# Kernel optimization log

Measured on AMD Instinct MI355X. Metric: run time of the kernel, lower is better.

Reference implementation:

```python
import jax, jax.numpy as jnp
import numpy as np

N = 100_000   # nodes
E = 1_600_000 # message-passing edges
EA = 1_000_000 # aux edges for bilinear head
G = 512       # graphs in batch
F_IN = 16     # num_node_features (fixed in source)
H = 32        # hidden_dim (fixed in source)


def setup_inputs() -> dict:
    key = jax.random.key(0)
    ks = jax.random.split(key, 8)
    x = jax.random.normal(ks[0], (N, F_IN), jnp.float32)
    edge_index = jax.random.randint(ks[1], (2, E), 0, N, dtype=jnp.int32)
    edge_index_aux = jax.random.randint(ks[2], (2, EA), 0, N, dtype=jnp.int32)
    batch = jnp.sort(jax.random.randint(ks[3], (N,), 0, G, dtype=jnp.int32))
    W1 = jax.random.normal(ks[4], (F_IN, H), jnp.float32) / np.sqrt(F_IN)
    b1 = jnp.zeros((H,), jnp.float32)
    W2 = jax.random.normal(ks[5], (H, H), jnp.float32) / np.sqrt(H)
    b2 = jnp.zeros((H,), jnp.float32)
    Wr = jax.random.normal(ks[6], (H, 1), jnp.float32) / np.sqrt(H)
    br = jnp.zeros((1,), jnp.float32)
    Wbil = jax.random.normal(ks[7], (1, H, H), jnp.float32) / H
    bbil = jnp.zeros((1,), jnp.float32)
    return dict(x=x, edge_index=edge_index, edge_index_aux=edge_index_aux,
                batch=batch, W1=W1, b1=b1, W2=W2, b2=b2, Wr=Wr, br=br,
                Wbil=Wbil, bbil=bbil)


def gcn_conv(x, W, b, src, dst):
    # PyG GCNConv: x' = D^{-1/2}(A+I)D^{-1/2} (x W) + b, deg includes self-loop
    xw = x @ W                                                   # [N,H]
    deg = jax.ops.segment_sum(jnp.ones((src.shape[0],), x.dtype), dst,
                              num_segments=N) + 1.0              # +1 self-loop
    dinv = jax.lax.rsqrt(deg)                                    # [N]
    coef = dinv[src] * dinv[dst]                                 # [E]
    agg = jax.ops.segment_sum(xw[src] * coef[:, None], dst, num_segments=N)
    agg = agg + xw * (dinv * dinv)[:, None]                      # self-loop msg
    return agg + b


def reference(x, edge_index, edge_index_aux, batch,
              W1, b1, W2, b2, Wr, br, Wbil, bbil):
    src, dst = edge_index[0], edge_index[1]
    h = jax.nn.relu(gcn_conv(x, W1, b1, src, dst))
    h = gcn_conv(h, W2, b2, src, dst)
    # global_mean_pool over graph ids
    cnt = jax.ops.segment_sum(jnp.ones((N,), h.dtype), batch, num_segments=G)
    pooled = jax.ops.segment_sum(h, batch, num_segments=G) / jnp.maximum(cnt, 1.0)[:, None]
    reg_output = pooled @ Wr + br                                # [G,1]
    # Bilinear edge head: out_e = x1_e^T W x2_e + b
    h1 = h[edge_index_aux[0]]                                    # [EA,H]
    h2 = h[edge_index_aux[1]]                                    # [EA,H]
    edge_pred = jnp.einsum('ei,ij,ej->e', h1, Wbil[0], h2)[:, None] + bbil
    return reg_output, edge_pred
```

## Files before the change

### kernel.cpp

```cpp
#include <hip/hip_runtime.h>
#include <hip/hip_bf16.h>
#include <string.h>
#include <stdint.h>

typedef __hip_bfloat16 bf16;

#define FIN 16
#define H   32
#define PADW 64
#define NB  512
#define BINCAP 4096
#define NPBMAX 200
#define PSTRIDE 65
#define CHUNK 4096
#define SCAN_CHUNK 1024
#define MAXSEG 64
#define POOLBLK 256

typedef int vi4 __attribute__((ext_vector_type(4)));

__device__ __forceinline__ float b2f(bf16 v) { return __bfloat162float(v); }

__device__ __forceinline__ float loadf(const void* p, size_t i, int f32) {
    return f32 ? ((const float*)p)[i] : b2f(((const bf16*)p)[i]);
}
__device__ __forceinline__ void storef(void* p, size_t i, float v, int f32) {
    if (f32) ((float*)p)[i] = v;
    else     ((bf16*)p)[i] = __float2bfloat16(v);
}

__device__ __forceinline__ unsigned pack2(float lo, float hi) {
    bf16 a = __float2bfloat16(lo), b = __float2bfloat16(hi);
    unsigned short ua, ub;
    memcpy(&ua, &a, 2); memcpy(&ub, &b, 2);
    return ((unsigned)ub << 16) | (unsigned)ua;
}
__device__ __forceinline__ float f_lo(unsigned u) {
    union { unsigned i; float f; } v; v.i = u << 16; return v.f;
}
__device__ __forceinline__ float f_hi(unsigned u) {
    union { unsigned i; float f; } v; v.i = u & 0xffff0000u; return v.f;
}

__global__ void k_detect(const void* __restrict__ x, int nelem, int* __restrict__ flag,
                         float* __restrict__ zf, int nzf,
                         int* __restrict__ zi, int nzi) {
    for (int i = threadIdx.x; i < nzf; i += blockDim.x) zf[i] = 0.f;
    if (zi) for (int i = threadIdx.x; i < nzi; i += blockDim.x) zi[i] = 0;
    __shared__ int cntS;
    if (threadIdx.x == 0) cntS = 0;
    __syncthreads();
    int bad = 0;
    const bf16* p = (const bf16*)x;
    for (int i = threadIdx.x; i < nelem; i += blockDim.x) {
        float v = b2f(p[i]);
        float a = fabsf(v);
        if (isnan(v) || a > 1024.f || (v != 0.f && a < 1e-20f)) bad++;
    }
    atomicAdd(&cntS, bad);
    __syncthreads();
    if (threadIdx.x == 0) flag[0] = (cntS > 64) ? 1 : 0;
}

__global__ void __launch_bounds__(1024) k_p1(
        const int* __restrict__ src, const int* __restrict__ dst,
        int* __restrict__ bincur, unsigned* __restrict__ binbuf,
        int E, int npb) {
    __shared__ int hcnt[4][NB];
    __shared__ int hbase[NB];
    __shared__ int scur[NB];
    int tid = threadIdx.x;
    int grp = tid >> 8;
    int e0 = blockIdx.x * CHUNK;
    int nE = E - e0;
    if (nE > CHUNK) nE = CHUNK;
    for (int i = tid; i < 4 * NB; i += blockDim.x) ((int*)hcnt)[i] = 0;
    __syncthreads();
    for (int i = tid; i < nE; i += blockDim.x)
        atomicAdd(&hcnt[grp][dst[e0 + i] / npb], 1);
    __syncthreads();
    for (int i = tid; i < NB; i += blockDim.x) {
        int c = hcnt[0][i] + hcnt[1][i] + hcnt[2][i] + hcnt[3][i];
        hbase[i] = c ? atomicAdd(&bincur[i], c) : 0;
        scur[i] = 0;
    }
    __syncthreads();
    for (int i = tid; i < nE; i += blockDim.x) {
        int d = dst[e0 + i];
        int bin = d / npb;
        int pos = hbase[bin] + atomicAdd(&scur[bin], 1);
        if (pos < BINCAP)
            binbuf[(size_t)bin * BINCAP + pos] =
                ((unsigned)src[e0 + i] << 10) | (unsigned)(d - bin * npb);
    }
}

__global__ void __launch_bounds__(256) k_p2x(
        const int* __restrict__ bincur, const unsigned* __restrict__ binbuf,
        int* __restrict__ csr, int* __restrict__ deg, float* __restrict__ dinv,
        const void* __restrict__ x, const void* __restrict__ W1,
        const int* __restrict__ flag, unsigned* __restrict__ xsb,
        int N, int npb) {
    __shared__ int cur[NPBMAX];
    __shared__ int psr[NPBMAX * PSTRIDE];
    __shared__ float sW1[FIN * H];
    int f32v = flag[0];
    int b = blockIdx.x;
    int base = b * npb;
    int nn = N - base;
    if (nn > npb) nn = npb;
    if (nn < 0) nn = 0;
    for (int i = threadIdx.x; i < FIN * H; i += blockDim.x) sW1[i] = loadf(W1, i, f32v);
    for (int i = threadIdx.x; i < nn; i += blockDim.x) cur[i] = 0;
    __syncthreads();
    int cnt = bincur[b];
    if (cnt > BINCAP) cnt = BINCAP;
    const unsigned* buf = binbuf + (size_t)b * BINCAP;
    for (int j = threadIdx.x; j < cnt; j += blockDim.x) {
        unsigned p = buf[j];
        int loc = (int)(p & 1023u);
        int s = (int)(p >> 10);
        int pos = atomicAdd(&cur[loc], 1);
        if (pos < PADW) psr[loc * PSTRIDE + pos] = s;
    }
    __syncthreads();
    int tot = nn * PADW;
    for (int idx = threadIdx.x; idx < tot; idx += blockDim.x) {
        int i = idx >> 6, p = idx & 63;
        int dg = cur[i];
        if (dg > PADW) dg = PADW;
        if (p < dg)
            csr[((size_t)(base + i) << 6) + p] = psr[i * PSTRIDE + p];
    }
    for (int i = threadIdx.x; i < nn; i += blockDim.x) {
        int dg = cur[i];
        int n = base + i;
        deg[n] = dg;
        float dv = rsqrtf((float)dg + 1.0f);
        dinv[n] = dv;
        float xr[FIN];
        if (f32v) {
            const float4* xp = (const float4*)((const float*)x + (size_t)n * FIN);
            float4 v0 = xp[0], v1 = xp[1], v2 = xp[2], v3 = xp[3];
            xr[0]=v0.x; xr[1]=v0.y; xr[2]=v0.z; xr[3]=v0.w;
            xr[4]=v1.x; xr[5]=v1.y; xr[6]=v1.z; xr[7]=v1.w;
            xr[8]=v2.x; xr[9]=v2.y; xr[10]=v2.z; xr[11]=v2.w;
            xr[12]=v3.x; xr[13]=v3.y; xr[14]=v3.z; xr[15]=v3.w;
        } else {
            const uint4* xp = (const uint4*)((const bf16*)x + (size_t)n * FIN);
            uint4 u0 = xp[0], u1 = xp[1];
            xr[0]=f_lo(u0.x); xr[1]=f_hi(u0.x); xr[2]=f_lo(u0.y); xr[3]=f_hi(u0.y);
            xr[4]=f_lo(u0.z); xr[5]=f_hi(u0.z); xr[6]=f_lo(u0.w); xr[7]=f_hi(u0.w);
            xr[8]=f_lo(u1.x); xr[9]=f_hi(u1.x); xr[10]=f_lo(u1.y); xr[11]=f_hi(u1.y);
            xr[12]=f_lo(u1.z); xr[13]=f_hi(u1.z); xr[14]=f_lo(u1.w); xr[15]=f_hi(u1.w);
        }
        unsigned outp[16];
#pragma unroll
        for (int jj = 0; jj < 16; jj++) {
            float s0 = 0.f, s1 = 0.f;
#pragma unroll
            for (int f = 0; f < FIN; f++) {
                float xv = xr[f];
                s0 += xv * sW1[f * H + 2 * jj];
                s1 += xv * sW1[f * H + 2 * jj + 1];
            }
            outp[jj] = pack2(s0 * dv, s1 * dv);
        }
        uint4* op = (uint4*)(xsb + (size_t)n * 16);
        op[0] = make_uint4(outp[0], outp[1], outp[2], outp[3]);
        op[1] = make_uint4(outp[4], outp[5], outp[6], outp[7]);
        op[2] = make_uint4(outp[8], outp[9], outp[10], outp[11]);
        op[3] = make_uint4(outp[12], outp[13], outp[14], outp[15]);
    }
}


__global__ void k_fillp(const int* __restrict__ src, const int* __restrict__ dst,
                        int* __restrict__ cursor, int* __restrict__ csr, int E) {
    int e = blockIdx.x * blockDim.x + threadIdx.x;
    if (e >= E) return;
    int d = dst[e];
    int pos = atomicAdd(&cursor[d], 1);
    if (pos < PADW) csr[((size_t)d << 6) + pos] = src[e];
}

__global__ void k_dinvi(const int* __restrict__ deg, float* __restrict__ dinv, int N) {
    int t = blockIdx.x * blockDim.x + threadIdx.x;
    if (t < N) dinv[t] = rsqrtf((float)deg[t] + 1.0f);
}

__global__ void __launch_bounds__(256) k_xw1v(
        const void* __restrict__ x, const void* __restrict__ W1,
        const float* __restrict__ dinv, const int* __restrict__ flag,
        unsigned* __restrict__ xsb, int N) {
    __shared__ float sW[FIN * H];
    __shared__ float sxx[16 * 17];
    int f32 = flag[0];
    for (int i = threadIdx.x; i < FIN * H; i += blockDim.x) sW[i] = loadf(W1, i, f32);
    __syncthreads();
    int t = blockIdx.x * blockDim.x + threadIdx.x;
    int n = t >> 4, j = t & 15, g = threadIdx.x >> 4;
    if (n < N) sxx[g * 17 + j] = loadf(x, (size_t)n * FIN + j, f32);
    __syncthreads();
    if (n >= N) return;
    float dv = dinv[n];
    float s0 = 0.f, s1 = 0.f;
    const float* xp = &sxx[g * 17];
#pragma unroll
    for (int i = 0; i < FIN; i++) {
        float xv = xp[i];
        s0 += xv * sW[i * H + 2 * j];
        s1 += xv * sW[i * H + 2 * j + 1];
    }
    xsb[(size_t)n * 16 + j] = pack2(s0 * dv, s1 * dv);
}

#define GACC8(TBL)                                                        \
    for (; k + 8 <= len; k += 8) {                                        \
        vi4 sA = *(const vi4*)(lst + k);                                  \
        vi4 sB = *(const vi4*)(lst + k + 4);                              \
        unsigned u0 = TBL[(size_t)sA.x * 16 + j];                         \
        unsigned u1 = TBL[(size_t)sA.y * 16 + j];                         \
        unsigned u2 = TBL[(size_t)sA.z * 16 + j];                         \
        unsigned u3 = TBL[(size_t)sA.w * 16 + j];                         \
        unsigned u4 = TBL[(size_t)sB.x * 16 + j];                         \
        unsigned u5 = TBL[(size_t)sB.y * 16 + j];                         \
        unsigned u6 = TBL[(size_t)sB.z * 16 + j];                         \
        unsigned u7 = TBL[(size_t)sB.w * 16 + j];                         \
        a0 += f_lo(u0); a1 += f_hi(u0);                                   \
        b0 += f_lo(u1); b1v += f_hi(u1);                                  \
        a0 += f_lo(u2); a1 += f_hi(u2);                                   \
        b0 += f_lo(u3); b1v += f_hi(u3);                                  \
        a0 += f_lo(u4); a1 += f_hi(u4);                                   \
        b0 += f_lo(u5); b1v += f_hi(u5);                                  \
        a0 += f_lo(u6); a1 += f_hi(u6);                                   \
        b0 += f_lo(u7); b1v += f_hi(u7);                                  \
    }                                                                     \
    for (; k + 4 <= len; k += 4) {                                        \
        vi4 s4 = *(const vi4*)(lst + k);                                  \
        unsigned u0 = TBL[(size_t)s4.x * 16 + j];                         \
        unsigned u1 = TBL[(size_t)s4.y * 16 + j];                         \
        unsigned u2 = TBL[(size_t)s4.z * 16 + j];                         \
        unsigned u3 = TBL[(size_t)s4.w * 16 + j];                         \
        a0 += f_lo(u0); a1 += f_hi(u0);                                   \
        b0 += f_lo(u1); b1v += f_hi(u1);                                  \
        a0 += f_lo(u2); a1 += f_hi(u2);                                   \
        b0 += f_lo(u3); b1v += f_hi(u3);                                  \
    }                                                                     \
    for (; k < len; k++) {                                                \
        unsigned u2 = TBL[(size_t)lst[k] * 16 + j];                       \
        a0 += f_lo(u2); a1 += f_hi(u2);                                   \
    }

__global__ void __launch_bounds__(256) k_g1(
        const int* __restrict__ deg, const int* __restrict__ csr,
        const float* __restrict__ dinv, const unsigned* __restrict__ xsb,
        const void* __restrict__ W2, const void* __restrict__ b1,
        const int* __restrict__ flag, unsigned* __restrict__ xsb2, int N) {
    __shared__ float sW[H * H];
    __shared__ float sb[H];
    __shared__ float shh[16 * 34];
    int f32 = flag[0];
    for (int i = threadIdx.x; i < H * H; i += blockDim.x) sW[i] = loadf(W2, i, f32);
    if (threadIdx.x < H) sb[threadIdx.x] = loadf(b1, threadIdx.x, f32);
    __syncthreads();
    int t = blockIdx.x * blockDim.x + threadIdx.x;
    int d = t >> 4, j = t & 15, g = threadIdx.x >> 4;
    float dv = 0.f;
    if (d < N) {
        int len = deg[d];
        if (len > PADW) len = PADW;
        const int* lst = csr + ((size_t)d << 6);
        unsigned u = xsb[(size_t)d * 16 + j];
        float a0 = f_lo(u), a1 = f_hi(u);
        float b0 = 0.f, b1v = 0.f;
        int k = 0;
        GACC8(xsb)
        dv = dinv[d];
        float h0 = (a0 + b0) * dv + sb[2 * j];
        float h1 = (a1 + b1v) * dv + sb[2 * j + 1];
        shh[g * 34 + 2 * j]     = h0 > 0.f ? h0 : 0.f;
        shh[g * 34 + 2 * j + 1] = h1 > 0.f ? h1 : 0.f;
    }
    __syncthreads();
    if (d >= N) return;
    float s0 = 0.f, s1 = 0.f;
    const float* hp = &shh[g * 34];
#pragma unroll
    for (int i = 0; i < H; i++) {
        float hv = hp[i];
        s0 += hv * sW[i * H + 2 * j];
        s1 += hv * sW[i * H + 2 * j + 1];
    }
    xsb2[(size_t)d * 16 + j] = pack2(s0 * dv, s1 * dv);
}

__global__ void __launch_bounds__(256) k_g2(
        const int* __restrict__ deg, const int* __restrict__ csr,
        const float* __restrict__ dinv, const unsigned* __restrict__ xsb2,
        const void* __restrict__ b2v, const void* __restrict__ Wbil,
        const int* __restrict__ batch, const int* __restrict__ flag,
        float* __restrict__ pooled, float* __restrict__ cnt,
        unsigned* __restrict__ hb, unsigned* __restrict__ gb, int N) {
    __shared__ float sW[H * H];
    __shared__ float sb[H];
    __shared__ float shh[16 * 34];
    __shared__ int   sg[16];
    __shared__ float spool[16 * H];
    __shared__ float scnt[16];
    int f32 = flag[0];
    int tid = threadIdx.x;
    for (int i = tid; i < H * H; i += blockDim.x) sW[i] = loadf(Wbil, i, f32);
    if (tid < H) sb[tid] = loadf(b2v, tid, f32);
    for (int i = tid; i < 16 * H; i += blockDim.x) spool[i] = 0.f;
    if (tid < 16) scnt[tid] = 0.f;
    int blk0 = blockIdx.x * 16;
    int nv = N - blk0;
    if (nv > 16) nv = 16;
    if (tid < nv) sg[tid] = batch[blk0 + tid];
    __syncthreads();
    int d = blk0 + (tid >> 4), j = tid & 15, g = tid >> 4;
    float h0 = 0.f, h1 = 0.f;
    int valid = (g < nv);
    if (valid) {
        int len = deg[d];
        if (len > PADW) len = PADW;
        const int* lst = csr + ((size_t)d << 6);
        unsigned u = xsb2[(size_t)d * 16 + j];
        float a0 = f_lo(u), a1 = f_hi(u);
        float b0 = 0.f, b1v = 0.f;
        int k = 0;
        GACC8(xsb2)
        float dv = dinv[d];
        h0 = (a0 + b0) * dv + sb[2 * j];
        h1 = (a1 + b1v) * dv + sb[2 * j + 1];
        hb[(size_t)d * 16 + j] = pack2(h0, h1);
        shh[g * 34 + 2 * j]     = h0;
        shh[g * 34 + 2 * j + 1] = h1;
    }
    int g0 = sg[0];
    int nseg = sg[nv - 1] - g0 + 1;
    if (valid) {
        int sgn = sg[g];
        if (nseg <= 16) {
            atomicAdd(&spool[(sgn - g0) * H + 2 * j], h0);
            atomicAdd(&spool[(sgn - g0) * H + 2 * j + 1], h1);
            if (j == 0) atomicAdd(&scnt[sgn - g0], 1.f);
        } else {
            atomicAdd(&pooled[(size_t)sgn * H + 2 * j], h0);
            atomicAdd(&pooled[(size_t)sgn * H + 2 * j + 1], h1);
            if (j == 0) atomicAdd(&cnt[sgn], 1.f);
        }
    }
    __syncthreads();
    if (nseg <= 16) {
        for (int i = tid; i < nseg * H; i += blockDim.x) {
            float v = spool[i];
            if (v != 0.f) atomicAdd(&pooled[(size_t)(g0 + (i >> 5)) * H + (i & 31)], v);
        }
        for (int i = tid; i < nseg; i += blockDim.x)
            if (scnt[i] != 0.f) atomicAdd(&cnt[g0 + i], scnt[i]);
    }
    if (!valid) return;
    float s0 = 0.f, s1 = 0.f;
    const float* hp = &shh[g * 34];
#pragma unroll
    for (int i = 0; i < H; i++) {
        float hv = hp[i];
        s0 += hv * sW[i * H + 2 * j];
        s1 += hv * sW[i * H + 2 * j + 1];
    }
    gb[(size_t)d * 16 + j] = pack2(s0, s1);
}

__global__ void __launch_bounds__(512) k_poolhb(
        const void* __restrict__ b2v, const void* __restrict__ Wbil,
        const int* __restrict__ batch, const int* __restrict__ flag,
        const float* __restrict__ aggB, float* __restrict__ pooled,
        float* __restrict__ cnt, bf16* __restrict__ hb, bf16* __restrict__ gb,
        int N) {
    __shared__ float sW[H * H];
    __shared__ float sb[H];
    __shared__ float sh[POOLBLK][H];
    __shared__ int   sg[POOLBLK];
    __shared__ float spool[MAXSEG * H];
    __shared__ float scnt[MAXSEG];
    int f32 = flag[0];
    int tid = threadIdx.x;
    for (int i = tid; i < H * H; i += blockDim.x) sW[i] = loadf(Wbil, i, f32);
    if (tid < H) sb[tid] = loadf(b2v, tid, f32);
    int blk0 = blockIdx.x * POOLBLK;
    int nvalid = N - blk0;
    if (nvalid > POOLBLK) nvalid = POOLBLK;
    if (tid < nvalid) sg[tid] = batch[blk0 + tid];
    for (int i = tid; i < MAXSEG * H; i += blockDim.x) spool[i] = 0.f;
    if (tid < MAXSEG) scnt[tid] = 0.f;
    __syncthreads();
    int f = tid & 31, k = tid >> 5;
    for (int r = k; r < nvalid; r += 16) {
        float v = aggB[(size_t)(blk0 + r) * H + f] + sb[f];
        sh[r][f] = v;
        hb[(size_t)(blk0 + r) * H + f] = __float2bfloat16(v);
    }
    __syncthreads();
    int g0 = sg[0];
    int nseg = sg[nvalid - 1] - g0 + 1;
    if (nseg <= MAXSEG) {
        for (int r = k; r < nvalid; r += 16) {
            int gl = sg[r] - g0;
            atomicAdd(&spool[gl * H + f], sh[r][f]);
            if (f == 0) atomicAdd(&scnt[gl], 1.f);
        }
    } else {
        for (int r = k; r < nvalid; r += 16) {
            atomicAdd(&pooled[(size_t)sg[r] * H + f], sh[r][f]);
            if (f == 0) atomicAdd(&cnt[sg[r]], 1.f);
        }
    }
    for (int r = k; r < nvalid; r += 16) {
        float s = 0.f;
#pragma unroll
        for (int i = 0; i < H; i++) s += sh[r][i] * sW[i * H + f];
        gb[(size_t)(blk0 + r) * H + f] = __float2bfloat16(s);
    }
    if (nseg <= MAXSEG) {
        __syncthreads();
        for (int i = tid; i < nseg * H; i += blockDim.x)
            atomicAdd(&pooled[(size_t)(g0 + (i >> 5)) * H + (i & 31)], spool[i]);
        for (int i = tid; i < nseg; i += blockDim.x)
            atomicAdd(&cnt[g0 + i], scnt[i]);
    }
}


__global__ void k_degi(const int* __restrict__ dst, int* __restrict__ deg, int E) {
    int t = blockIdx.x * blockDim.x + threadIdx.x;
    if (t < E) atomicAdd(&deg[dst[t]], 1);
}

__global__ void k_scan1(const int* __restrict__ deg, int* __restrict__ partials, int N) {
    __shared__ int sd[256];
    int base = blockIdx.x * SCAN_CHUNK + threadIdx.x * 4;
    int s = 0;
#pragma unroll
    for (int k = 0; k < 4; k++) { int i = base + k; s += (i < N) ? deg[i] : 0; }
    sd[threadIdx.x] = s;
    __syncthreads();
    for (int off = 128; off > 0; off >>= 1) {
        if (threadIdx.x < off) sd[threadIdx.x] += sd[threadIdx.x + off];
        __syncthreads();
    }
    if (threadIdx.x == 0) partials[blockIdx.x] = sd[0];
}

__global__ void k_scan2(const int* __restrict__ partials, int* __restrict__ chunk_off, int B1) {
    __shared__ int sd[256];
    int t = threadIdx.x;
    int lv[4];
    int s = 0;
#pragma unroll
    for (int k = 0; k < 4; k++) { int i = t * 4 + k; lv[k] = (i < B1) ? partials[i] : 0; s += lv[k]; }
    sd[t] = s;
    __syncthreads();
    int inc = s;
    for (int off = 1; off < 256; off <<= 1) {
        int v = (t >= off) ? sd[t - off] : 0;
        __syncthreads();
        sd[t] += v;
        __syncthreads();
    }
    int run = sd[t] - inc;
#pragma unroll
    for (int k = 0; k < 4; k++) { int i = t * 4 + k; if (i < B1) chunk_off[i] = run; run += lv[k]; }
    if (t == 255) chunk_off[B1] = run;
}

__global__ void k_scan3(const int* __restrict__ deg, const int* __restrict__ chunk_off,
                        int* __restrict__ row_ptr, int* __restrict__ cursor,
                        int N, int E) {
    __shared__ int sd[256];
    int t = threadIdx.x;
    int base = blockIdx.x * SCAN_CHUNK + t * 4;
    int lv[4];
    int s = 0;
#pragma unroll
    for (int k = 0; k < 4; k++) { int i = base + k; lv[k] = (i < N) ? deg[i] : 0; s += lv[k]; }
    sd[t] = s;
    __syncthreads();
    int inc = s;
    for (int off = 1; off < 256; off <<= 1) {
        int v = (t >= off) ? sd[t - off] : 0;
        __syncthreads();
        sd[t] += v;
        __syncthreads();
    }
    int run = chunk_off[blockIdx.x] + sd[t] - inc;
#pragma unroll
    for (int k = 0; k < 4; k++) {
        int i = base + k;
        if (i < N) { row_ptr[i] = run; cursor[i] = run; }
        run += lv[k];
    }
    if (blockIdx.x == 0 && t == 0) row_ptr[N] = E;
}

__global__ void k_fill(const int* __restrict__ src, const int* __restrict__ dst,
                       int* __restrict__ cursor, int* __restrict__ csr, int E) {
    int e = blockIdx.x * blockDim.x + threadIdx.x;
    if (e >= E) return;
    int pos = atomicAdd(&cursor[dst[e]], 1);
    csr[pos] = src[e];
}

__global__ void k_gather(const int* __restrict__ row_ptr, const int* __restrict__ csr,
                         const float* __restrict__ dinv, const float* __restrict__ xs,
                         float* __restrict__ agg, int N) {
    int t = blockIdx.x * blockDim.x + threadIdx.x;
    int d = t >> 5, f = t & 31;
    if (d >= N) return;
    int beg = row_ptr[d], end = row_ptr[d + 1];
    float acc  = xs[(size_t)d * H + f];
    float acc2 = 0.f;
    int j = beg;
    for (; j + 1 < end; j += 2) {
        int s0 = csr[j], s1 = csr[j + 1];
        acc  += xs[(size_t)s0 * H + f];
        acc2 += xs[(size_t)s1 * H + f];
    }
    if (j < end) acc += xs[(size_t)csr[j] * H + f];
    agg[(size_t)d * H + f] = (acc + acc2) * dinv[d];
}

__global__ void k_xw1n(const void* __restrict__ x, const void* __restrict__ W1,
                       const float* __restrict__ dinv, const int* __restrict__ flag,
                       float* __restrict__ xs, int N) {
    __shared__ float sW[FIN * H];
    int f32 = flag[0];
    for (int i = threadIdx.x; i < FIN * H; i += blockDim.x) sW[i] = loadf(W1, i, f32);
    __syncthreads();
    int n = blockIdx.x * blockDim.x + threadIdx.x;
    if (n >= N) return;
    float xr[FIN];
#pragma unroll
    for (int i = 0; i < FIN; i++) xr[i] = loadf(x, (size_t)n * FIN + i, f32);
    float dv = dinv[n];
#pragma unroll
    for (int f = 0; f < H; f++) {
        float s = 0.f;
#pragma unroll
        for (int i = 0; i < FIN; i++) s += xr[i] * sW[i * H + f];
        xs[(size_t)n * H + f] = s * dv;
    }
}

__global__ void k_h1xw2n(const void* __restrict__ W2, const void* __restrict__ b1,
                         const float* __restrict__ dinv, const int* __restrict__ flag,
                         const float* __restrict__ agg, float* __restrict__ xs2, int N) {
    __shared__ float sW[H * H];
    __shared__ float sb[H];
    int f32 = flag[0];
    for (int i = threadIdx.x; i < H * H; i += blockDim.x) sW[i] = loadf(W2, i, f32);
    if (threadIdx.x < H) sb[threadIdx.x] = loadf(b1, threadIdx.x, f32);
    __syncthreads();
    int n = blockIdx.x * blockDim.x + threadIdx.x;
    if (n >= N) return;
    float hr[H];
#pragma unroll
    for (int f = 0; f < H; f++) {
        float v = agg[(size_t)n * H + f] + sb[f];
        hr[f] = v > 0.f ? v : 0.f;
    }
    float dv = dinv[n];
#pragma unroll
    for (int f = 0; f < H; f++) {
        float s = 0.f;
#pragma unroll
        for (int i = 0; i < H; i++) s += hr[i] * sW[i * H + f];
        xs2[(size_t)n * H + f] = s * dv;
    }
}


__global__ void k_degf(const int* __restrict__ dst, float* __restrict__ deg, int E) {
    int t = blockIdx.x * blockDim.x + threadIdx.x;
    if (t < E) atomicAdd(&deg[dst[t]], 1.0f);
}
__global__ void k_dinvf(float* __restrict__ deg, int N) {
    int t = blockIdx.x * blockDim.x + threadIdx.x;
    if (t < N) deg[t] = rsqrtf(deg[t] + 1.0f);
}
__global__ void k_xw1o(const void* __restrict__ x, const void* __restrict__ W1,
                       const float* __restrict__ dinv, const int* __restrict__ flag,
                       float* __restrict__ xw, float* __restrict__ agg, int N) {
    __shared__ float sW[FIN * H];
    int f32 = flag[0];
    for (int i = threadIdx.x; i < FIN * H; i += blockDim.x) sW[i] = loadf(W1, i, f32);
    __syncthreads();
    int n = blockIdx.x * blockDim.x + threadIdx.x;
    if (n >= N) return;
    float xr[FIN];
#pragma unroll
    for (int i = 0; i < FIN; i++) xr[i] = loadf(x, (size_t)n * FIN + i, f32);
    float dv = dinv[n], dv2 = dv * dv;
#pragma unroll
    for (int f = 0; f < H; f++) {
        float s = 0.f;
#pragma unroll
        for (int i = 0; i < FIN; i++) s += xr[i] * sW[i * H + f];
        xw[(size_t)n * H + f]  = s;
        agg[(size_t)n * H + f] = s * dv2;
    }
}
__global__ void k_scatter(const int* __restrict__ src, const int* __restrict__ dst,
                          const float* __restrict__ dinv, const float* __restrict__ xw,
                          float* __restrict__ agg, int E) {
    int t = blockIdx.x * blockDim.x + threadIdx.x;
    int e = t >> 5, f = t & 31;
    if (e >= E) return;
    int s = src[e], d = dst[e];
    float c = dinv[s] * dinv[d];
    atomicAdd(&agg[(size_t)d * H + f], xw[(size_t)s * H + f] * c);
}
__global__ void k_h1xw2o(const void* __restrict__ W2, const void* __restrict__ b1,
                         const float* __restrict__ dinv, const int* __restrict__ flag,
                         float* __restrict__ aggio, float* __restrict__ xw2, int N) {
    __shared__ float sW[H * H];
    __shared__ float sb[H];
    int f32 = flag[0];
    for (int i = threadIdx.x; i < H * H; i += blockDim.x) sW[i] = loadf(W2, i, f32);
    if (threadIdx.x < H) sb[threadIdx.x] = loadf(b1, threadIdx.x, f32);
    __syncthreads();
    int n = blockIdx.x * blockDim.x + threadIdx.x;
    if (n >= N) return;
    float hr[H];
#pragma unroll
    for (int f = 0; f < H; f++) {
        float v = aggio[(size_t)n * H + f] + sb[f];
        hr[f] = v > 0.f ? v : 0.f;
    }
    float dv = dinv[n], dv2 = dv * dv;
#pragma unroll
    for (int f = 0; f < H; f++) {
        float s = 0.f;
#pragma unroll
        for (int i = 0; i < H; i++) s += hr[i] * sW[i * H + f];
        xw2[(size_t)n * H + f]   = s;
        aggio[(size_t)n * H + f] = s * dv2;
    }
}


__global__ void k_bilreg(const int* __restrict__ srcA, const int* __restrict__ dstA,
                         const unsigned* __restrict__ gb32, const unsigned* __restrict__ hb32,
                         const void* __restrict__ bbil,
                         const float* __restrict__ pooled, const float* __restrict__ cnt,
                         const void* __restrict__ Wr, const void* __restrict__ br,
                         const int* __restrict__ flag, void* __restrict__ out,
                         int G, int EA) {
    int f32 = flag[0];
    int t = blockIdx.x * blockDim.x + threadIdx.x;
    if (t < EA) {
        int s = srcA[t], d = dstA[t];
        const uint4* gp = (const uint4*)(gb32 + (size_t)s * (H / 2));
        const uint4* hp = (const uint4*)(hb32 + (size_t)d * (H / 2));
        float acc = 0.f;
#pragma unroll
        for (int kk = 0; kk < 4; kk++) {
            uint4 a = gp[kk], b = hp[kk];
            acc += f_lo(a.x) * f_lo(b.x) + f_hi(a.x) * f_hi(b.x);
            acc += f_lo(a.y) * f_lo(b.y) + f_hi(a.y) * f_hi(b.y);
            acc += f_lo(a.z) * f_lo(b.z) + f_hi(a.z) * f_hi(b.z);
            acc += f_lo(a.w) * f_lo(b.w) + f_hi(a.w) * f_hi(b.w);
        }
        storef(out, (size_t)G + t, acc + loadf(bbil, 0, f32), f32);
    } else {
        int g = t - EA;
        if (g < G) {
            float c = cnt[g];
            c = c > 1.f ? c : 1.f;
            float s = 0.f;
#pragma unroll
            for (int i = 0; i < H; i++) s += pooled[(size_t)g * H + i] * loadf(Wr, i, f32);
            storef(out, g, s / c + loadf(br, 0, f32), f32);
        }
    }
}

extern "C" void kernel_launch(void* const* d_in, const int* in_sizes, int n_in,
                              void* d_out, int out_size, void* d_ws, size_t ws_size,
                              hipStream_t stream) {
    const void* x     = d_in[0];
    const int*  ei    = (const int*)d_in[1];
    const int*  eia   = (const int*)d_in[2];
    const int*  batch = (const int*)d_in[3];
    const void* W1    = d_in[4];
    const void* b1    = d_in[5];
    const void* W2    = d_in[6];
    const void* b2    = d_in[7];
    const void* Wr    = d_in[8];
    const void* br    = d_in[9];
    const void* Wbil  = d_in[10];
    const void* bbil  = d_in[11];

    const int N  = in_sizes[0] / FIN;
    const int E  = in_sizes[1] / 2;
    const int EA = in_sizes[2] / 2;
    const int G  = out_size - EA;

    float* ws     = (float*)d_ws;
    int*   flag   = (int*)ws;
    float* dinv   = ws + 16;
    float* A      = dinv + N;
    float* B      = A + (size_t)N * H;
    float* pooled = B + (size_t)N * H;
    float* cnt    = pooled + (size_t)G * H;
    float* fend   = cnt + G;

    unsigned* xsb  = (unsigned*)B;
    unsigned* xsb2 = (unsigned*)B + (size_t)N * 16;
    unsigned* hb32 = (unsigned*)A;
    unsigned* gb32 = hb32 + (size_t)N * (H / 2);

    int* degA   = (int*)fend;
    int* csrA   = (int*)(((uintptr_t)(degA + N) + 15) & ~(uintptr_t)15);
    int* bincur = csrA + (size_t)N * PADW;
    size_t needA  = (size_t)((char*)bincur - (char*)d_ws);
    size_t needA2 = (size_t)((char*)(bincur + NB) - (char*)d_ws);
    const int B1 = (N + SCAN_CHUNK - 1) / SCAN_CHUNK;
    int* deg_i     = (int*)fend;
    int* curB      = deg_i + N;
    int* row_ptr   = curB + N;
    int* chunk_off = row_ptr + N + 1;
    int* csrB      = chunk_off + B1 + 1;
    size_t needB = (size_t)((char*)(csrB + E) - (char*)d_ws);

    const int npb = (N + NB - 1) / NB;
    const bool tierA2 = (ws_size >= needA2) && (npb <= NPBMAX) && (N <= (1 << 22)) &&
                        ((size_t)NB * BINCAP <= (size_t)N * H * 2);
    const bool tierA  = !tierA2 && (ws_size >= needA);
    const bool tierB  = !tierA2 && !tierA && (ws_size >= needB) && (B1 <= 1024);

    const int* src  = ei;
    const int* dst  = ei + E;
    const int* srcA = eia;
    const int* dstA = eia + EA;

    const int TB = 256;
    const int npool = G * H + G;

    k_detect<<<1, 1024, 0, stream>>>(x, 1024, flag, pooled, npool,
                                     (tierA2 || tierA) ? bincur : (int*)nullptr,
                                     tierA2 ? NB : 0);

    int ggrid16 = (int)(((long)N * 16 + TB - 1) / TB);
    int ggrid32 = (int)(((long)N * 32 + TB - 1) / TB);
    int ngrid   = (N + TB - 1) / TB;

    if (tierA2) {
        unsigned* binbuf = (unsigned*)A;
        int nblk1 = (E + CHUNK - 1) / CHUNK;
        k_p1<<<nblk1, 1024, 0, stream>>>(src, dst, bincur, binbuf, E, npb);
        k_p2x<<<NB, TB, 0, stream>>>(bincur, binbuf, csrA, degA, dinv,
                                     x, W1, flag, xsb, N, npb);
        k_g1<<<ggrid16, TB, 0, stream>>>(degA, csrA, dinv, xsb, W2, b1, flag, xsb2, N);
        k_g2<<<ggrid16, TB, 0, stream>>>(degA, csrA, dinv, xsb2, b2, Wbil, batch, flag,
                                         pooled, cnt, hb32, gb32, N);
    } else if (tierA) {
        hipMemsetAsync(degA, 0, (size_t)N * sizeof(int), stream);
        k_fillp<<<(E + TB - 1) / TB, TB, 0, stream>>>(src, dst, degA, csrA, E);
        k_dinvi<<<ngrid, TB, 0, stream>>>(degA, dinv, N);
        k_xw1v<<<ggrid16, TB, 0, stream>>>(x, W1, dinv, flag, xsb, N);
        k_g1<<<ggrid16, TB, 0, stream>>>(degA, csrA, dinv, xsb, W2, b1, flag, xsb2, N);
        k_g2<<<ggrid16, TB, 0, stream>>>(degA, csrA, dinv, xsb2, b2, Wbil, batch, flag,
                                         pooled, cnt, hb32, gb32, N);
    } else if (tierB) {
        hipMemsetAsync(deg_i, 0, (size_t)N * sizeof(int), stream);
        k_degi<<<(E + TB - 1) / TB, TB, 0, stream>>>(dst, deg_i, E);
        k_dinvi<<<ngrid, TB, 0, stream>>>(deg_i, dinv, N);
        k_scan1<<<B1, TB, 0, stream>>>(deg_i, chunk_off, N);
        k_scan2<<<1, TB, 0, stream>>>(chunk_off, chunk_off, B1);
        k_scan3<<<B1, TB, 0, stream>>>(deg_i, chunk_off, row_ptr, curB, N, E);
        k_fill<<<(E + TB - 1) / TB, TB, 0, stream>>>(src, dst, curB, csrB, E);
        k_xw1n<<<ngrid, TB, 0, stream>>>(x, W1, dinv, flag, A, N);
        k_gather<<<ggrid32, TB, 0, stream>>>(row_ptr, csrB, dinv, A, B, N);
        k_h1xw2n<<<ngrid, TB, 0, stream>>>(W2, b1, dinv, flag, B, A, N);
        k_gather<<<ggrid32, TB, 0, stream>>>(row_ptr, csrB, dinv, A, B, N);
        k_poolhb<<<(N + POOLBLK - 1) / POOLBLK, 512, 0, stream>>>(
            b2, Wbil, batch, flag, B, pooled, cnt, (bf16*)hb32, (bf16*)gb32, N);
    } else {
        hipMemsetAsync(dinv, 0, (size_t)N * sizeof(float), stream);
        k_degf<<<(E + TB - 1) / TB, TB, 0, stream>>>(dst, dinv, E);
        k_dinvf<<<ngrid, TB, 0, stream>>>(dinv, N);
        k_xw1o<<<ngrid, TB, 0, stream>>>(x, W1, dinv, flag, A, B, N);
        long tot = (long)E * 32;
        int sgrid = (int)((tot + TB - 1) / TB);
        k_scatter<<<sgrid, TB, 0, stream>>>(src, dst, dinv, A, B, E);
        k_h1xw2o<<<ngrid, TB, 0, stream>>>(W2, b1, dinv, flag, B, A, N);
        k_scatter<<<sgrid, TB, 0, stream>>>(src, dst, dinv, A, B, E);
        k_poolhb<<<(N + POOLBLK - 1) / POOLBLK, 512, 0, stream>>>(
            b2, Wbil, batch, flag, B, pooled, cnt, (bf16*)hb32, (bf16*)gb32, N);
    }

    k_bilreg<<<(EA + G + TB - 1) / TB, TB, 0, stream>>>(
        srcA, dstA, gb32, hb32, bbil, pooled, cnt, Wr, br, flag, d_out, G, EA);
}
```

Before: 263.9 us.

## Pad bin counters, halve binning chunk, vectorize CSR writes, widen zero-init grid

Bin counters are spaced 16 ints apart so global atomics from binning blocks no longer contend on shared cache lines, and the edge chunk per binning block is halved to launch more blocks. CSR rows are written as 4-int vectors instead of scalars. The zeroing kernel now runs on 8 blocks, and the dinv load is moved ahead of the gather loop so its latency overlaps. The cost is more workspace for counters and more global atomics from the larger number of binning blocks.

```diff
diff --git a/kernel.cpp b/kernel.cpp
--- a/kernel.cpp
+++ b/kernel.cpp
@@ -12,7 +12,8 @@
 #define BINCAP 4096
 #define NPBMAX 200
 #define PSTRIDE 65
-#define CHUNK 4096
+#define CHUNK 2048
+#define BINSTRIDE 16
 #define SCAN_CHUNK 1024
 #define MAXSEG 64
 #define POOLBLK 256
@@ -45,8 +46,11 @@
 __global__ void k_detect(const void* __restrict__ x, int nelem, int* __restrict__ flag,
                          float* __restrict__ zf, int nzf,
                          int* __restrict__ zi, int nzi) {
-    for (int i = threadIdx.x; i < nzf; i += blockDim.x) zf[i] = 0.f;
-    if (zi) for (int i = threadIdx.x; i < nzi; i += blockDim.x) zi[i] = 0;
+    int gt = blockIdx.x * blockDim.x + threadIdx.x;
+    int gs = gridDim.x * blockDim.x;
+    for (int i = gt; i < nzf; i += gs) zf[i] = 0.f;
+    if (zi) for (int i = gt; i < nzi; i += gs) zi[i] = 0;
+    if (blockIdx.x != 0) return;
     __shared__ int cntS;
     if (threadIdx.x == 0) cntS = 0;
     __syncthreads();
@@ -81,7 +85,7 @@
     __syncthreads();
     for (int i = tid; i < NB; i += blockDim.x) {
         int c = hcnt[0][i] + hcnt[1][i] + hcnt[2][i] + hcnt[3][i];
-        hbase[i] = c ? atomicAdd(&bincur[i], c) : 0;
+        hbase[i] = c ? atomicAdd(&bincur[i * BINSTRIDE], c) : 0;
         scur[i] = 0;
     }
     __syncthreads();
@@ -113,7 +117,7 @@
     for (int i = threadIdx.x; i < FIN * H; i += blockDim.x) sW1[i] = loadf(W1, i, f32v);
     for (int i = threadIdx.x; i < nn; i += blockDim.x) cur[i] = 0;
     __syncthreads();
-    int cnt = bincur[b];
+    int cnt = bincur[b * BINSTRIDE];
     if (cnt > BINCAP) cnt = BINCAP;
     const unsigned* buf = binbuf + (size_t)b * BINCAP;
     for (int j = threadIdx.x; j < cnt; j += blockDim.x) {
@@ -124,13 +128,16 @@
         if (pos < PADW) psr[loc * PSTRIDE + pos] = s;
     }
     __syncthreads();
-    int tot = nn * PADW;
-    for (int idx = threadIdx.x; idx < tot; idx += blockDim.x) {
-        int i = idx >> 6, p = idx & 63;
+    int tot4 = nn * 16;
+    for (int idx = threadIdx.x; idx < tot4; idx += blockDim.x) {
+        int i = idx >> 4, p4 = (idx & 15) << 2;
         int dg = cur[i];
         if (dg > PADW) dg = PADW;
-        if (p < dg)
-            csr[((size_t)(base + i) << 6) + p] = psr[i * PSTRIDE + p];
+        if (p4 < dg) {
+            const int* pr = &psr[i * PSTRIDE + p4];
+            vi4 v = {pr[0], pr[1], pr[2], pr[3]};
+            *(vi4*)(csr + ((size_t)(base + i) << 6) + p4) = v;
+        }
     }
     for (int i = threadIdx.x; i < nn; i += blockDim.x) {
         int dg = cur[i];
@@ -270,13 +277,13 @@
     if (d < N) {
         int len = deg[d];
         if (len > PADW) len = PADW;
+        dv = dinv[d];
         const int* lst = csr + ((size_t)d << 6);
         unsigned u = xsb[(size_t)d * 16 + j];
         float a0 = f_lo(u), a1 = f_hi(u);
         float b0 = 0.f, b1v = 0.f;
         int k = 0;
         GACC8(xsb)
-        dv = dinv[d];
         float h0 = (a0 + b0) * dv + sb[2 * j];
         float h1 = (a1 + b1v) * dv + sb[2 * j + 1];
         shh[g * 34 + 2 * j]     = h0 > 0.f ? h0 : 0.f;
@@ -325,13 +332,13 @@
     if (valid) {
         int len = deg[d];
         if (len > PADW) len = PADW;
+        float dv = dinv[d];
         const int* lst = csr + ((size_t)d << 6);
         unsigned u = xsb2[(size_t)d * 16 + j];
         float a0 = f_lo(u), a1 = f_hi(u);
         float b0 = 0.f, b1v = 0.f;
         int k = 0;
         GACC8(xsb2)
-        float dv = dinv[d];
         h0 = (a0 + b0) * dv + sb[2 * j];
         h1 = (a1 + b1v) * dv + sb[2 * j + 1];
         hb[(size_t)d * 16 + j] = pack2(h0, h1);
@@ -725,7 +732,7 @@
     int* csrA   = (int*)(((uintptr_t)(degA + N) + 15) & ~(uintptr_t)15);
     int* bincur = csrA + (size_t)N * PADW;
     size_t needA  = (size_t)((char*)bincur - (char*)d_ws);
-    size_t needA2 = (size_t)((char*)(bincur + NB) - (char*)d_ws);
+    size_t needA2 = (size_t)((char*)(bincur + NB * BINSTRIDE) - (char*)d_ws);
     const int B1 = (N + SCAN_CHUNK - 1) / SCAN_CHUNK;
     int* deg_i     = (int*)fend;
     int* curB      = deg_i + N;
@@ -748,9 +755,9 @@
     const int TB = 256;
     const int npool = G * H + G;
 
-    k_detect<<<1, 1024, 0, stream>>>(x, 1024, flag, pooled, npool,
-                                     (tierA2 || tierA) ? bincur : (int*)nullptr,
-                                     tierA2 ? NB : 0);
+    k_detect<<<8, 1024, 0, stream>>>(x, 1024, flag, pooled, npool,
+                                     tierA2 ? bincur : (int*)nullptr,
+                                     tierA2 ? NB * BINSTRIDE : 0);
 
     int ggrid16 = (int)(((long)N * 16 + TB - 1) / TB);
     int ggrid32 = (int)(((long)N * 32 + TB - 1) / TB);
```

Result: no change. 264.6 us (+0.3%).
